# Kernel tuning notes

Hardware: AMD Instinct MI355X
Metric: run time of the kernel (lower is better)

## Reference

```python
import jax, jax.numpy as jnp
import numpy as np

B, C, T = 8, 512, 2048
INTER = C // 2            # inter_channels default = in_channels // 2
L = 2                     # temporal_layer_num


def _pos_encoding(c, t):
    # standard sinusoidal PE, returned as (c, t) to match pos().permute(0,2,1)
    pos = jnp.arange(t, dtype=jnp.float32)[:, None]            # (t,1)
    i = jnp.arange(0, c, 2, dtype=jnp.float32)                 # (c/2,)
    div = jnp.exp(-(jnp.log(10000.0) / c) * i)                 # (c/2,)
    pe = jnp.zeros((t, c), dtype=jnp.float32)
    pe = pe.at[:, 0::2].set(jnp.sin(pos * div))
    pe = pe.at[:, 1::2].set(jnp.cos(pos * div))
    return pe.T                                                # (c,t)


def _conv1x1(w, b, x):
    # kernel_size=1 Conv1d == channel GEMM: w (o,c), x (b,c,t) -> (b,o,t)
    return jnp.einsum('oc,bct->bot', w, x) + b[:, None]


def _temporal_conv(x, w, d):
    # Conv2d(1, c, kernel=(3, c), dilation=(d,1), padding=(d,0), no bias)
    # x (b,c,t) -> input (b,1,t,c); kernel w (c,3,c) -> (c,1,3,c); out (b,c,t,1)
    x4 = x.transpose(0, 2, 1)[:, None, :, :]
    k = w[:, None, :, :]
    y = jax.lax.conv_general_dilated(
        x4, k, window_strides=(1, 1), padding=((d, d), (0, 0)),
        rhs_dilation=(d, 1), dimension_numbers=('NCHW', 'OIHW', 'NCHW'))
    return y[..., 0]                                           # (b,c,t)


def setup_inputs() -> dict:
    key = jax.random.key(0)
    ks = jax.random.split(key, 12)
    n = lambda k, shape, s=0.02: jax.random.normal(k, shape, jnp.float32) * s
    return {
        'x': jax.random.normal(ks[0], (B, C, T), jnp.float32),
        'w_tr': n(ks[1], (C, C)),
        'b_tr': jnp.zeros((C,), jnp.float32),
        'w_tc': n(ks[2], (L, C, 3, C), 0.001),   # init.normal_(std=0.001)
        'w_g': n(ks[3], (L + 1, INTER, C)),
        'b_g': jnp.zeros((L + 1, INTER), jnp.float32),
        'w_th': n(ks[4], (L + 1, INTER, C)),
        'b_th': jnp.zeros((L + 1, INTER), jnp.float32),
        'w_ph': n(ks[5], (L + 1, INTER, C)),
        'b_ph': jnp.zeros((L + 1, INTER), jnp.float32),
        'w_W': n(ks[6], (C, INTER * (L + 1))),
        'b_W': jnp.zeros((C,), jnp.float32),
        'gamma': 1.0 + n(ks[7], (C,)),
        'beta': n(ks[8], (C,)),
    }


def reference(x, w_tr, b_tr, w_tc, w_g, b_g, w_th, b_th, w_ph, b_ph,
              w_W, b_W, gamma, beta):
    b, c, t = x.shape
    x = x + _pos_encoding(c, t)[None]                 # add positional encoding
    x = jax.nn.relu(_conv1x1(w_tr, b_tr, x))          # tranpos_w + relu

    # temporal dilated-conv features, then raw x as last branch
    temps = [_temporal_conv(x, w_tc[i], i + 1) for i in range(w_tc.shape[0])]
    temps.append(x)

    ys = []
    for i, tx in enumerate(temps):
        gx = _conv1x1(w_g[i], b_g[i], tx)             # (b,inter,t)
        th = _conv1x1(w_th[i], b_th[i], tx)           # (b,inter,t)
        ph = _conv1x1(w_ph[i], b_ph[i], tx)           # (b,inter,t)
        f = jax.nn.softmax(jnp.einsum('bit,bis->bts', th, ph), axis=-1)
        ys.append(jnp.einsum('bts,bis->bit', f, gx))  # (b,inter,t)

    y = jnp.concatenate(ys, axis=1)                   # (b, 3*inter, t)
    wy = _conv1x1(w_W, b_W, y)                        # (b,c,t)
    # BatchNorm1d, training-mode batch stats over (batch, time)
    mean = wy.mean(axis=(0, 2), keepdims=True)
    var = wy.var(axis=(0, 2), keepdims=True)
    wy = (wy - mean) * jax.lax.rsqrt(var + 1e-5)
    wy = wy * gamma[None, :, None] + beta[None, :, None]
    return wy + x
```

## Files before the change

### kernel.cpp

```cpp
#include <hip/hip_runtime.h>

#define B_ 8
#define C_ 512
#define T_ 2048
#define I_ 256

typedef _Float16 f16x8 __attribute__((ext_vector_type(8)));
typedef float f32x4 __attribute__((ext_vector_type(4)));
typedef unsigned short u16;
typedef unsigned short u16x4 __attribute__((ext_vector_type(4)));

__device__ __forceinline__ u16 f2h(float f) {
    _Float16 h = (_Float16)f;
    return *(u16*)&h;
}
__device__ __forceinline__ float h2f(u16 u) {
    _Float16 h = *(_Float16*)&u;
    return (float)h;
}

#define AS1 __attribute__((address_space(1)))
#define AS3 __attribute__((address_space(3)))
__device__ __forceinline__ void gload16(const u16* g, u16* l) {
    __builtin_amdgcn_global_load_lds((const AS1 void*)(const void*)g,
                                     (AS3 void*)(void*)l, 16, 0, 0);
}

template <int WMODE, bool BIAS, bool RELU>
__global__ __launch_bounds__(256) void mfma_gemm(
    const u16* __restrict__ A, long aB, int aZdiv, int lda,
    const u16* __restrict__ Bm, long bB, int ldb,
    const float* __restrict__ bias, int biasStride,
    float* __restrict__ Cf, u16* __restrict__ Cn, long cB, int ldc,
    u16* __restrict__ Ct, long ctB, int ldct, int ctOff,
    int K)
{
    __shared__ u16 sA[128 * 64];
    __shared__ u16 sB[128 * 64];
    const int z = blockIdx.z;
    const int zw = z / aZdiv;
    const int m0 = blockIdx.y * 128, n0 = blockIdx.x * 128;
    const int tid = threadIdx.x;
    const int lane = tid & 63, wv = tid >> 6;
    const int wm = wv >> 1, wn = wv & 1;
    const int l15 = lane & 15, l4 = lane >> 4;

    const u16* Ab = A + (long)zw * aB + (long)m0 * lda;
    const u16* Bb = Bm + (long)z * bB + (long)n0 * ldb;

    const int srow = wv * 32 + (lane >> 3);
    const int sk16 = (lane & 7) ^ (lane >> 3);

    f32x4 acc[4][4];
    #pragma unroll
    for (int i = 0; i < 4; ++i)
        #pragma unroll
        for (int j = 0; j < 4; ++j) acc[i][j] = (f32x4){0.f, 0.f, 0.f, 0.f};

    for (int k0 = 0; k0 < K; k0 += 64) {
        #pragma unroll
        for (int ch = 0; ch < 4; ++ch) {
            gload16(Ab + (long)(srow + ch * 8) * lda + k0 + sk16 * 8,
                    &sA[wv * 2048 + ch * 512]);
            gload16(Bb + (long)(srow + ch * 8) * ldb + k0 + sk16 * 8,
                    &sB[wv * 2048 + ch * 512]);
        }
        __syncthreads();
        #pragma unroll
        for (int kk = 0; kk < 2; ++kk) {
            f16x8 af[4], bfr[4];
            #pragma unroll
            for (int f = 0; f < 4; ++f) {
                const int ra = wm * 64 + f * 16 + l15;
                af[f] = *(const f16x8*)&sA[ra * 64 + ((((kk << 2) | l4) ^ (ra & 7)) << 3)];
                const int rb = wn * 64 + f * 16 + l15;
                bfr[f] = *(const f16x8*)&sB[rb * 64 + ((((kk << 2) | l4) ^ (rb & 7)) << 3)];
            }
            #pragma unroll
            for (int mi = 0; mi < 4; ++mi)
                #pragma unroll
                for (int ni = 0; ni < 4; ++ni)
                    acc[mi][ni] = __builtin_amdgcn_mfma_f32_16x16x32_f16(
                        af[mi], bfr[ni], acc[mi][ni], 0, 0, 0);
        }
        __syncthreads();
    }

    #pragma unroll
    for (int mi = 0; mi < 4; ++mi) {
        const int mb = m0 + wm * 64 + mi * 16 + l4 * 4;
        float bv[4] = {0.f, 0.f, 0.f, 0.f};
        if (BIAS) {
            const float* bp = bias + (long)zw * biasStride;
            #pragma unroll
            for (int r = 0; r < 4; ++r) bv[r] = bp[mb + r];
        }
        #pragma unroll
        for (int ni = 0; ni < 4; ++ni) {
            const int nb = n0 + wn * 64 + ni * 16 + l15;
            float v[4];
            #pragma unroll
            for (int r = 0; r < 4; ++r) {
                v[r] = acc[mi][ni][r] + bv[r];
                if (RELU) v[r] = fmaxf(v[r], 0.f);
            }
            if (WMODE & 1) {
                #pragma unroll
                for (int r = 0; r < 4; ++r)
                    Cf[(long)z * cB + (long)(mb + r) * ldc + nb] = v[r];
            }
            if (WMODE & 2) {
                #pragma unroll
                for (int r = 0; r < 4; ++r)
                    Cn[(long)z * cB + (long)(mb + r) * ldc + nb] = f2h(v[r]);
            }
            if (WMODE & 4) {
                u16x4 pk;
                #pragma unroll
                for (int r = 0; r < 4; ++r) pk[r] = f2h(v[r]);
                *(u16x4*)&Ct[(long)z * ctB + (long)nb * ldct + ctOff + mb] = pk;
            }
        }
    }
}

__global__ __launch_bounds__(512) void flash_attn(
    const u16* __restrict__ thA, const u16* __restrict__ phA,
    const u16* __restrict__ gxA, u16* __restrict__ YT)
{
    __shared__ u16 sK[64 * 256];
    __shared__ u16 sV[256 * 64];
    __shared__ u16 sP[8 * 16 * 64];

    const int flat = blockIdx.y * 16 + blockIdx.x;
    const int swz = (flat & 7) * 48 + (flat >> 3);
    const int qb = swz & 15, z = swz >> 4;
    const int br = z >> 3, b = z & 7;
    const int t0 = qb * 128;
    const int tid = threadIdx.x;
    const int lane = tid & 63, wv = tid >> 6;
    const int l15 = lane & 15, l4 = lane >> 4;

    const u16* Qz = thA + (long)z * (T_ * I_);
    const u16* Kz = phA + (long)z * (T_ * I_);
    const u16* Vz = gxA + (long)z * ((long)I_ * T_);

    f16x8 qf[8];
    {
        const u16* qrow = Qz + (long)(t0 + wv * 16 + l15) * I_ + l4 * 8;
        #pragma unroll
        for (int ks = 0; ks < 8; ++ks) qf[ks] = *(const f16x8*)(qrow + ks * 32);
    }

    f32x4 oacc[16];
    #pragma unroll
    for (int i = 0; i < 16; ++i) oacc[i] = (f32x4){0.f, 0.f, 0.f, 0.f};
    float mrun[4] = {-1e30f, -1e30f, -1e30f, -1e30f};
    float lrun[4] = {0.f, 0.f, 0.f, 0.f};

    const int krow = tid >> 5;
    const int kk16 = (tid & 31) ^ (krow & 7);
    const int vrow = tid >> 3;
    const int vk16 = (tid & 7) ^ (vrow & 7);

    for (int s0 = 0; s0 < T_; s0 += 64) {
        #pragma unroll
        for (int is = 0; is < 4; ++is) {
            gload16(Kz + (long)(s0 + is * 16 + krow) * I_ + kk16 * 8,
                    &sK[is * 4096 + tid * 8]);
            gload16(Vz + (long)(is * 64 + vrow) * T_ + s0 + vk16 * 8,
                    &sV[is * 4096 + tid * 8]);
        }
        __syncthreads();

        f32x4 sacc[4];
        #pragma unroll
        for (int nf = 0; nf < 4; ++nf) sacc[nf] = (f32x4){0.f, 0.f, 0.f, 0.f};
        #pragma unroll
        for (int nf = 0; nf < 4; ++nf) {
            const int srow = nf * 16 + l15;
            #pragma unroll
            for (int ks = 0; ks < 8; ++ks) {
                f16x8 kf = *(const f16x8*)&sK[srow * 256 + ((((ks << 2) | l4) ^ (srow & 7)) << 3)];
                sacc[nf] = __builtin_amdgcn_mfma_f32_16x16x32_f16(qf[ks], kf, sacc[nf], 0, 0, 0);
            }
        }

        float scale[4];
        #pragma unroll
        for (int r = 0; r < 4; ++r) {
            float v0 = fmaxf(fmaxf(sacc[0][r], sacc[1][r]),
                             fmaxf(sacc[2][r], sacc[3][r]));
            #pragma unroll
            for (int o = 8; o; o >>= 1) v0 = fmaxf(v0, __shfl_xor(v0, o, 64));
            const float mnew = fmaxf(mrun[r], v0);
            scale[r] = __expf(mrun[r] - mnew);
            mrun[r] = mnew;
        }
        float rsum[4] = {0.f, 0.f, 0.f, 0.f};
        #pragma unroll
        for (int nf = 0; nf < 4; ++nf) {
            #pragma unroll
            for (int r = 0; r < 4; ++r) {
                const float p = __expf(sacc[nf][r] - mrun[r]);
                rsum[r] += p;
                const int tl = l4 * 4 + r;
                const int sl = l15 + nf * 16;
                sP[wv * 1024 + tl * 64 + ((((sl >> 3) ^ (tl & 7)) << 3) | (sl & 7))] = f2h(p);
            }
        }
        #pragma unroll
        for (int r = 0; r < 4; ++r) {
            #pragma unroll
            for (int o = 8; o; o >>= 1) rsum[r] += __shfl_xor(rsum[r], o, 64);
            lrun[r] = lrun[r] * scale[r] + rsum[r];
        }
        #pragma unroll
        for (int nf = 0; nf < 16; ++nf)
            #pragma unroll
            for (int r = 0; r < 4; ++r) oacc[nf][r] *= scale[r];

        f16x8 pa[2];
        #pragma unroll
        for (int kk = 0; kk < 2; ++kk)
            pa[kk] = *(const f16x8*)&sP[wv * 1024 + l15 * 64 + ((((kk << 2) | l4) ^ (l15 & 7)) << 3)];
        #pragma unroll
        for (int nf = 0; nf < 16; ++nf) {
            const int dvr = nf * 16 + l15;
            #pragma unroll
            for (int kk = 0; kk < 2; ++kk) {
                f16x8 vf = *(const f16x8*)&sV[dvr * 64 + ((((kk << 2) | l4) ^ (dvr & 7)) << 3)];
                oacc[nf] = __builtin_amdgcn_mfma_f32_16x16x32_f16(pa[kk], vf, oacc[nf], 0, 0, 0);
            }
        }
        __syncthreads();
    }

    #pragma unroll
    for (int r = 0; r < 4; ++r) {
        const float inv = 1.f / lrun[r];
        const int t = t0 + wv * 16 + l4 * 4 + r;
        u16* dst = YT + ((long)b * T_ + t) * (3 * I_) + br * I_ + l15;
        #pragma unroll
        for (int nf = 0; nf < 16; ++nf)
            dst[nf * 16] = f2h(oacc[nf][r] * inv);
    }
}

__global__ __launch_bounds__(256) void to_f16(
    const float* __restrict__ s, u16* __restrict__ d, long n4)
{
    const long i = (long)blockIdx.x * 256 + threadIdx.x;
    if (i >= n4) return;
    const float4 v = ((const float4*)s)[i];
    u16x4 pk = {f2h(v.x), f2h(v.y), f2h(v.z), f2h(v.w)};
    ((u16x4*)d)[i] = pk;
}

__global__ __launch_bounds__(256) void peT_kernel(float* __restrict__ peT)
{
    const int idx = blockIdx.x * 256 + threadIdx.x;
    const int c = idx & (C_ - 1), t = idx >> 9;
    const float i2 = (float)(c & ~1);
    const float freq = expf(-(9.210340371976184f / (float)C_) * i2);
    const float ang = (float)t * freq;
    peT[idx] = (c & 1) ? cosf(ang) : sinf(ang);
}

__global__ __launch_bounds__(256) void xpose_add(
    const float* __restrict__ x, const float* __restrict__ peT,
    u16* __restrict__ xpeT)
{
    __shared__ float tile[64][65];
    const int b = blockIdx.z;
    const int t0 = blockIdx.x * 64, c0 = blockIdx.y * 64;
    const int rr = threadIdx.x >> 4, cc4 = (threadIdx.x & 15) << 2;
    #pragma unroll
    for (int p = 0; p < 4; ++p) {
        const int row = rr + p * 16;
        const float4 v = *(const float4*)&x[((long)b * C_ + c0 + row) * T_ + t0 + cc4];
        tile[row][cc4 + 0] = v.x; tile[row][cc4 + 1] = v.y;
        tile[row][cc4 + 2] = v.z; tile[row][cc4 + 3] = v.w;
    }
    __syncthreads();
    #pragma unroll
    for (int p = 0; p < 4; ++p) {
        const int tt = rr + p * 16;
        const int gt = t0 + tt;
        const float4 pv = *(const float4*)&peT[(long)gt * C_ + c0 + cc4];
        u16x4 pk = {f2h(tile[cc4 + 0][tt] + pv.x),
                    f2h(tile[cc4 + 1][tt] + pv.y),
                    f2h(tile[cc4 + 2][tt] + pv.z),
                    f2h(tile[cc4 + 3][tt] + pv.w)};
        *(u16x4*)&xpeT[((long)b * T_ + gt) * C_ + c0 + cc4] = pk;
    }
}

__global__ __launch_bounds__(256) void build_bpt(
    const u16* __restrict__ x1T, u16* __restrict__ BpT, int d)
{
    const long i8 = (long)blockIdx.x * 256 + threadIdx.x;
    const long flat = i8 << 3;
    const int col = (int)(flat % (3 * C_));
    const long rest = flat / (3 * C_);
    const int t = (int)(rest & (T_ - 1));
    const int b = (int)(rest >> 11);
    const int kh = col >> 9;
    const int c = col & (C_ - 1);
    const int ts = t + (kh - 1) * d;
    uint4 v = make_uint4(0u, 0u, 0u, 0u);
    if ((unsigned)ts < (unsigned)T_)
        v = *(const uint4*)&x1T[((long)b * T_ + ts) * C_ + c];
    *(uint4*)&BpT[flat] = v;
}

__global__ __launch_bounds__(256) void stats_kernel(
    const float* __restrict__ wy, float* __restrict__ mean,
    float* __restrict__ rstd)
{
    __shared__ float sm[8];
    const int o = blockIdx.x, tid = threadIdx.x;
    float s = 0.f, ss = 0.f;
    for (int idx = tid; idx < B_ * T_; idx += 256) {
        const int b = idx >> 11, t = idx & (T_ - 1);
        const float vv = wy[((long)b * C_ + o) * T_ + t];
        s += vv; ss += vv * vv;
    }
    #pragma unroll
    for (int off = 32; off; off >>= 1) {
        s += __shfl_xor(s, off, 64);
        ss += __shfl_xor(ss, off, 64);
    }
    if ((tid & 63) == 0) { sm[tid >> 6] = s; sm[4 + (tid >> 6)] = ss; }
    __syncthreads();
    if (tid == 0) {
        s = sm[0] + sm[1] + sm[2] + sm[3];
        ss = sm[4] + sm[5] + sm[6] + sm[7];
        const float mu = s / (float)(B_ * T_);
        const float var = ss / (float)(B_ * T_) - mu * mu;
        mean[o] = mu;
        rstd[o] = rsqrtf(var + 1e-5f);
    }
}

__global__ __launch_bounds__(256) void final_kernel(
    float* __restrict__ out, const u16* __restrict__ x1n,
    const float* __restrict__ mean, const float* __restrict__ rstd,
    const float* __restrict__ gamma, const float* __restrict__ beta)
{
    const long i4 = (long)blockIdx.x * 256 + threadIdx.x;
    const long i = i4 * 4;
    const int c = (int)((i / T_) & (C_ - 1));
    const float4 w = ((const float4*)out)[i4];
    const uint2 xv = ((const uint2*)x1n)[i4];
    const u16* xb = (const u16*)&xv;
    const float mu = mean[c];
    const float a = rstd[c] * gamma[c];
    const float bb = beta[c];
    float4 r;
    r.x = (w.x - mu) * a + bb + h2f(xb[0]);
    r.y = (w.y - mu) * a + bb + h2f(xb[1]);
    r.z = (w.z - mu) * a + bb + h2f(xb[2]);
    r.w = (w.w - mu) * a + bb + h2f(xb[3]);
    ((float4*)out)[i4] = r;
}

extern "C" void kernel_launch(void* const* d_in, const int* in_sizes, int n_in,
                              void* d_out, int out_size, void* d_ws, size_t ws_size,
                              hipStream_t stream)
{
    const float* x    = (const float*)d_in[0];
    const float* w_tr = (const float*)d_in[1];
    const float* b_tr = (const float*)d_in[2];
    const float* w_tc = (const float*)d_in[3];
    const float* w_g  = (const float*)d_in[4];
    const float* b_g  = (const float*)d_in[5];
    const float* w_th = (const float*)d_in[6];
    const float* b_th = (const float*)d_in[7];
    const float* w_ph = (const float*)d_in[8];
    const float* b_ph = (const float*)d_in[9];
    const float* w_W  = (const float*)d_in[10];
    const float* b_W  = (const float*)d_in[11];
    const float* gamma = (const float*)d_in[12];
    const float* beta  = (const float*)d_in[13];
    float* out = (float*)d_out;

    char* pp = (char*)d_ws;
    auto nextp = [&](long bytes) { char* r = pp; pp += (bytes + 255) & ~255L; return r; };
    const long TC = (long)T_ * C_;
    const long CT = (long)C_ * T_;
    const long TI = (long)T_ * I_;
    const long IT = (long)I_ * T_;

    float* peT  = (float*)nextp(4L * T_ * C_);
    u16* xpeT   = (u16*)nextp(2L * B_ * TC);
    u16* x1n    = (u16*)nextp(2L * B_ * CT);
    u16* txAll  = (u16*)nextp(2L * 3 * B_ * TC);
    u16* BpT    = (u16*)nextp(2L * B_ * T_ * 3 * C_);
    u16* gxAll  = (u16*)nextp(2L * 3 * B_ * IT);
    u16* thAll  = (u16*)nextp(2L * 3 * B_ * TI);
    u16* phAll  = (u16*)nextp(2L * 3 * B_ * TI);
    u16* YT     = (u16*)nextp(2L * B_ * T_ * 3 * I_);
    u16* w_trb  = (u16*)nextp(2L * C_ * C_);
    u16* w_tcb  = (u16*)nextp(2L * 2 * C_ * 3 * C_);
    u16* w_gb   = (u16*)nextp(2L * 3 * I_ * C_);
    u16* w_thb  = (u16*)nextp(2L * 3 * I_ * C_);
    u16* w_phb  = (u16*)nextp(2L * 3 * I_ * C_);
    u16* w_Wb   = (u16*)nextp(2L * C_ * 3 * I_);
    float* meanb = (float*)nextp(4L * C_);
    float* rstdb = (float*)nextp(4L * C_);

    u16* x1T = txAll + 2L * B_ * TC;

    auto cvt = [&](const float* s, u16* d, long n) {
        to_f16<<<(int)((n / 4 + 255) / 256), 256, 0, stream>>>(s, d, n / 4);
    };
    cvt(w_tr, w_trb, (long)C_ * C_);
    cvt(w_tc, w_tcb, 2L * C_ * 3 * C_);
    cvt(w_g,  w_gb,  3L * I_ * C_);
    cvt(w_th, w_thb, 3L * I_ * C_);
    cvt(w_ph, w_phb, 3L * I_ * C_);
    cvt(w_W,  w_Wb,  (long)C_ * 3 * I_);

    peT_kernel<<<(T_ * C_) / 256, 256, 0, stream>>>(peT);
    xpose_add<<<dim3(T_ / 64, C_ / 64, B_), 256, 0, stream>>>(x, peT, xpeT);

    mfma_gemm<6, true, true><<<dim3(16, 4, 8), 256, 0, stream>>>(
        w_trb, 0, 1, C_, xpeT, TC, C_, b_tr, 0,
        nullptr, x1n, CT, T_, x1T, TC, C_, 0, C_);

    build_bpt<<<(int)(B_ * T_ * 3 * C_ / 8 / 256), 256, 0, stream>>>(x1T, BpT, 1);
    mfma_gemm<4, false, false><<<dim3(16, 4, 8), 256, 0, stream>>>(
        w_tcb, 0, 1, 3 * C_, BpT, 3 * TC, 3 * C_, nullptr, 0,
        nullptr, nullptr, 0, 0, txAll, TC, C_, 0, 3 * C_);
    build_bpt<<<(int)(B_ * T_ * 3 * C_ / 8 / 256), 256, 0, stream>>>(x1T, BpT, 2);
    mfma_gemm<4, false, false><<<dim3(16, 4, 8), 256, 0, stream>>>(
        w_tcb + (long)C_ * 3 * C_, 0, 1, 3 * C_, BpT, 3 * TC, 3 * C_, nullptr, 0,
        nullptr, nullptr, 0, 0, txAll + (long)B_ * TC, TC, C_, 0, 3 * C_);

    mfma_gemm<2, true, false><<<dim3(16, 2, 24), 256, 0, stream>>>(
        w_gb, (long)I_ * C_, 8, C_, txAll, TC, C_, b_g, I_,
        nullptr, gxAll, IT, T_, nullptr, 0, 0, 0, C_);
    mfma_gemm<4, true, false><<<dim3(16, 2, 24), 256, 0, stream>>>(
        w_thb, (long)I_ * C_, 8, C_, txAll, TC, C_, b_th, I_,
        nullptr, nullptr, 0, 0, thAll, TI, I_, 0, C_);
    mfma_gemm<4, true, false><<<dim3(16, 2, 24), 256, 0, stream>>>(
        w_phb, (long)I_ * C_, 8, C_, txAll, TC, C_, b_ph, I_,
        nullptr, nullptr, 0, 0, phAll, TI, I_, 0, C_);

    flash_attn<<<dim3(16, 24), 512, 0, stream>>>(thAll, phAll, gxAll, YT);

    mfma_gemm<1, true, false><<<dim3(16, 4, 8), 256, 0, stream>>>(
        w_Wb, 0, 1, 3 * I_, YT, 3 * TI, 3 * I_, b_W, 0,
        out, nullptr, CT, T_, nullptr, 0, 0, 0, 3 * I_);

    stats_kernel<<<C_, 256, 0, stream>>>(out, meanb, rstdb);
    final_kernel<<<(int)(B_ * C_ * T_ / 4 / 256), 256, 0, stream>>>(
        out, x1n, meanb, rstdb, gamma, beta);
}
```

Baseline: 539.9 us.

## Fuse im2col into temporal-conv GEMM via padded slabs; widen flash-attn per-wave rows

The dilated temporal conv no longer materializes a 3x-wide im2col buffer (build_bpt). The GEMM instead reads row-shifted tiles straight from a zero-padded (T+4)-row x1 slab, and every activation buffer moves to that padded layout. Flash attention drops to 256 threads, with each wave handling 32 query rows so each K/V fragment feeds two MFMAs. It also gains setprio hints and a launch bound that allows two blocks per CU. The cost is higher register pressure in attention and an extra memset for the padding.

```diff
diff --git a/kernel.cpp b/kernel.cpp
--- a/kernel.cpp
+++ b/kernel.cpp
@@ -4,6 +4,7 @@
 #define C_ 512
 #define T_ 2048
 #define I_ 256
+#define TP_ (T_ + 4)
 
 typedef _Float16 f16x8 __attribute__((ext_vector_type(8)));
 typedef float f32x4 __attribute__((ext_vector_type(4)));
@@ -26,14 +27,14 @@
                                      (AS3 void*)(void*)l, 16, 0, 0);
 }
 
-template <int WMODE, bool BIAS, bool RELU>
+template <int WMODE, bool BIAS, bool RELU, bool TCONV>
 __global__ __launch_bounds__(256) void mfma_gemm(
     const u16* __restrict__ A, long aB, int aZdiv, int lda,
     const u16* __restrict__ Bm, long bB, int ldb,
     const float* __restrict__ bias, int biasStride,
     float* __restrict__ Cf, u16* __restrict__ Cn, long cB, int ldc,
     u16* __restrict__ Ct, long ctB, int ldct, int ctOff,
-    int K)
+    int K, int dShift)
 {
     __shared__ u16 sA[128 * 64];
     __shared__ u16 sB[128 * 64];
@@ -58,11 +59,18 @@
         for (int j = 0; j < 4; ++j) acc[i][j] = (f32x4){0.f, 0.f, 0.f, 0.f};
 
     for (int k0 = 0; k0 < K; k0 += 64) {
+        int bCol = k0;
+        int rOff = 0;
+        if (TCONV) {
+            const int kh = k0 >> 9;
+            rOff = (kh - 1) * dShift;
+            bCol = k0 & 511;
+        }
         #pragma unroll
         for (int ch = 0; ch < 4; ++ch) {
             gload16(Ab + (long)(srow + ch * 8) * lda + k0 + sk16 * 8,
                     &sA[wv * 2048 + ch * 512]);
-            gload16(Bb + (long)(srow + ch * 8) * ldb + k0 + sk16 * 8,
+            gload16(Bb + (long)(srow + ch * 8 + rOff) * ldb + bCol + sk16 * 8,
                     &sB[wv * 2048 + ch * 512]);
         }
         __syncthreads();
@@ -124,13 +132,13 @@
     }
 }
 
-__global__ __launch_bounds__(512) void flash_attn(
+__global__ __launch_bounds__(256, 2) void flash_attn(
     const u16* __restrict__ thA, const u16* __restrict__ phA,
     const u16* __restrict__ gxA, u16* __restrict__ YT)
 {
     __shared__ u16 sK[64 * 256];
     __shared__ u16 sV[256 * 64];
-    __shared__ u16 sP[8 * 16 * 64];
+    __shared__ u16 sP[4 * 32 * 64];
 
     const int flat = blockIdx.y * 16 + blockIdx.x;
     const int swz = (flat & 7) * 48 + (flat >> 3);
@@ -145,106 +153,126 @@
     const u16* Kz = phA + (long)z * (T_ * I_);
     const u16* Vz = gxA + (long)z * ((long)I_ * T_);
 
-    f16x8 qf[8];
-    {
-        const u16* qrow = Qz + (long)(t0 + wv * 16 + l15) * I_ + l4 * 8;
-        #pragma unroll
-        for (int ks = 0; ks < 8; ++ks) qf[ks] = *(const f16x8*)(qrow + ks * 32);
-    }
-
-    f32x4 oacc[16];
-    #pragma unroll
-    for (int i = 0; i < 16; ++i) oacc[i] = (f32x4){0.f, 0.f, 0.f, 0.f};
-    float mrun[4] = {-1e30f, -1e30f, -1e30f, -1e30f};
-    float lrun[4] = {0.f, 0.f, 0.f, 0.f};
-
-    const int krow = tid >> 5;
-    const int kk16 = (tid & 31) ^ (krow & 7);
-    const int vrow = tid >> 3;
-    const int vk16 = (tid & 7) ^ (vrow & 7);
+    f16x8 qf[2][8];
+    #pragma unroll
+    for (int m = 0; m < 2; ++m) {
+        const u16* qrow = Qz + (long)(t0 + wv * 32 + m * 16 + l15) * I_ + l4 * 8;
+        #pragma unroll
+        for (int ks = 0; ks < 8; ++ks) qf[m][ks] = *(const f16x8*)(qrow + ks * 32);
+    }
+
+    f32x4 oacc[2][16];
+    #pragma unroll
+    for (int m = 0; m < 2; ++m)
+        #pragma unroll
+        for (int i = 0; i < 16; ++i) oacc[m][i] = (f32x4){0.f, 0.f, 0.f, 0.f};
+    float mrun[2][4], lrun[2][4];
+    #pragma unroll
+    for (int m = 0; m < 2; ++m)
+        #pragma unroll
+        for (int r = 0; r < 4; ++r) { mrun[m][r] = -1e30f; lrun[m][r] = 0.f; }
 
     for (int s0 = 0; s0 < T_; s0 += 64) {
         #pragma unroll
-        for (int is = 0; is < 4; ++is) {
-            gload16(Kz + (long)(s0 + is * 16 + krow) * I_ + kk16 * 8,
-                    &sK[is * 4096 + tid * 8]);
-            gload16(Vz + (long)(is * 64 + vrow) * T_ + s0 + vk16 * 8,
-                    &sV[is * 4096 + tid * 8]);
+        for (int rr = 0; rr < 8; ++rr) {
+            const int fk = rr * 256 + tid;
+            const int ksr = fk >> 5, kslot = fk & 31;
+            gload16(Kz + (long)(s0 + ksr) * I_ + ((kslot ^ (ksr & 7)) << 3),
+                    &sK[fk * 8]);
+            const int dv = fk >> 3, vslot = fk & 7;
+            gload16(Vz + (long)dv * T_ + s0 + ((vslot ^ (dv & 7)) << 3),
+                    &sV[fk * 8]);
         }
         __syncthreads();
 
-        f32x4 sacc[4];
-        #pragma unroll
-        for (int nf = 0; nf < 4; ++nf) sacc[nf] = (f32x4){0.f, 0.f, 0.f, 0.f};
+        f32x4 sacc[2][4];
+        #pragma unroll
+        for (int m = 0; m < 2; ++m)
+            #pragma unroll
+            for (int nf = 0; nf < 4; ++nf) sacc[m][nf] = (f32x4){0.f, 0.f, 0.f, 0.f};
+        __builtin_amdgcn_s_setprio(1);
         #pragma unroll
         for (int nf = 0; nf < 4; ++nf) {
             const int srow = nf * 16 + l15;
             #pragma unroll
             for (int ks = 0; ks < 8; ++ks) {
                 f16x8 kf = *(const f16x8*)&sK[srow * 256 + ((((ks << 2) | l4) ^ (srow & 7)) << 3)];
-                sacc[nf] = __builtin_amdgcn_mfma_f32_16x16x32_f16(qf[ks], kf, sacc[nf], 0, 0, 0);
-            }
-        }
-
-        float scale[4];
-        #pragma unroll
-        for (int r = 0; r < 4; ++r) {
-            float v0 = fmaxf(fmaxf(sacc[0][r], sacc[1][r]),
-                             fmaxf(sacc[2][r], sacc[3][r]));
-            #pragma unroll
-            for (int o = 8; o; o >>= 1) v0 = fmaxf(v0, __shfl_xor(v0, o, 64));
-            const float mnew = fmaxf(mrun[r], v0);
-            scale[r] = __expf(mrun[r] - mnew);
-            mrun[r] = mnew;
-        }
-        float rsum[4] = {0.f, 0.f, 0.f, 0.f};
-        #pragma unroll
-        for (int nf = 0; nf < 4; ++nf) {
+                sacc[0][nf] = __builtin_amdgcn_mfma_f32_16x16x32_f16(qf[0][ks], kf, sacc[0][nf], 0, 0, 0);
+                sacc[1][nf] = __builtin_amdgcn_mfma_f32_16x16x32_f16(qf[1][ks], kf, sacc[1][nf], 0, 0, 0);
+            }
+        }
+        __builtin_amdgcn_s_setprio(0);
+
+        #pragma unroll
+        for (int m = 0; m < 2; ++m) {
+            float scale[4];
             #pragma unroll
             for (int r = 0; r < 4; ++r) {
-                const float p = __expf(sacc[nf][r] - mrun[r]);
-                rsum[r] += p;
-                const int tl = l4 * 4 + r;
-                const int sl = l15 + nf * 16;
-                sP[wv * 1024 + tl * 64 + ((((sl >> 3) ^ (tl & 7)) << 3) | (sl & 7))] = f2h(p);
-            }
-        }
-        #pragma unroll
-        for (int r = 0; r < 4; ++r) {
-            #pragma unroll
-            for (int o = 8; o; o >>= 1) rsum[r] += __shfl_xor(rsum[r], o, 64);
-            lrun[r] = lrun[r] * scale[r] + rsum[r];
-        }
-        #pragma unroll
-        for (int nf = 0; nf < 16; ++nf)
-            #pragma unroll
-            for (int r = 0; r < 4; ++r) oacc[nf][r] *= scale[r];
-
-        f16x8 pa[2];
-        #pragma unroll
-        for (int kk = 0; kk < 2; ++kk)
-            pa[kk] = *(const f16x8*)&sP[wv * 1024 + l15 * 64 + ((((kk << 2) | l4) ^ (l15 & 7)) << 3)];
+                float v0 = fmaxf(fmaxf(sacc[m][0][r], sacc[m][1][r]),
+                                 fmaxf(sacc[m][2][r], sacc[m][3][r]));
+                #pragma unroll
+                for (int o = 8; o; o >>= 1) v0 = fmaxf(v0, __shfl_xor(v0, o, 64));
+                const float mnew = fmaxf(mrun[m][r], v0);
+                scale[r] = __expf(mrun[m][r] - mnew);
+                mrun[m][r] = mnew;
+            }
+            float rsum[4] = {0.f, 0.f, 0.f, 0.f};
+            #pragma unroll
+            for (int nf = 0; nf < 4; ++nf) {
+                #pragma unroll
+                for (int r = 0; r < 4; ++r) {
+                    const float p = __expf(sacc[m][nf][r] - mrun[m][r]);
+                    rsum[r] += p;
+                    const int tl = m * 16 + l4 * 4 + r;
+                    const int sl = l15 + nf * 16;
+                    sP[wv * 2048 + tl * 64 + ((((sl >> 3) ^ (tl & 7)) << 3) | (sl & 7))] = f2h(p);
+                }
+            }
+            #pragma unroll
+            for (int r = 0; r < 4; ++r) {
+                #pragma unroll
+                for (int o = 8; o; o >>= 1) rsum[r] += __shfl_xor(rsum[r], o, 64);
+                lrun[m][r] = lrun[m][r] * scale[r] + rsum[r];
+            }
+            #pragma unroll
+            for (int nf = 0; nf < 16; ++nf)
+                #pragma unroll
+                for (int r = 0; r < 4; ++r) oacc[m][nf][r] *= scale[r];
+        }
+
+        f16x8 pa[2][2];
+        #pragma unroll
+        for (int m = 0; m < 2; ++m)
+            #pragma unroll
+            for (int kk = 0; kk < 2; ++kk)
+                pa[m][kk] = *(const f16x8*)&sP[wv * 2048 + (m * 16 + l15) * 64 +
+                                               ((((kk << 2) | l4) ^ (l15 & 7)) << 3)];
+        __builtin_amdgcn_s_setprio(1);
         #pragma unroll
         for (int nf = 0; nf < 16; ++nf) {
             const int dvr = nf * 16 + l15;
             #pragma unroll
             for (int kk = 0; kk < 2; ++kk) {
                 f16x8 vf = *(const f16x8*)&sV[dvr * 64 + ((((kk << 2) | l4) ^ (dvr & 7)) << 3)];
-                oacc[nf] = __builtin_amdgcn_mfma_f32_16x16x32_f16(pa[kk], vf, oacc[nf], 0, 0, 0);
-            }
-        }
+                oacc[0][nf] = __builtin_amdgcn_mfma_f32_16x16x32_f16(pa[0][kk], vf, oacc[0][nf], 0, 0, 0);
+                oacc[1][nf] = __builtin_amdgcn_mfma_f32_16x16x32_f16(pa[1][kk], vf, oacc[1][nf], 0, 0, 0);
+            }
+        }
+        __builtin_amdgcn_s_setprio(0);
         __syncthreads();
     }
 
     #pragma unroll
-    for (int r = 0; r < 4; ++r) {
-        const float inv = 1.f / lrun[r];
-        const int t = t0 + wv * 16 + l4 * 4 + r;
-        u16* dst = YT + ((long)b * T_ + t) * (3 * I_) + br * I_ + l15;
-        #pragma unroll
-        for (int nf = 0; nf < 16; ++nf)
-            dst[nf * 16] = f2h(oacc[nf][r] * inv);
-    }
+    for (int m = 0; m < 2; ++m)
+        #pragma unroll
+        for (int r = 0; r < 4; ++r) {
+            const float inv = 1.f / lrun[m][r];
+            const int t = t0 + wv * 32 + m * 16 + l4 * 4 + r;
+            u16* dst = YT + ((long)b * T_ + t) * (3 * I_) + br * I_ + l15;
+            #pragma unroll
+            for (int nf = 0; nf < 16; ++nf)
+                dst[nf * 16] = f2h(oacc[m][nf][r] * inv);
+        }
 }
 
 __global__ __launch_bounds__(256) void to_f16(
@@ -294,24 +322,6 @@
                     f2h(tile[cc4 + 3][tt] + pv.w)};
         *(u16x4*)&xpeT[((long)b * T_ + gt) * C_ + c0 + cc4] = pk;
     }
-}
-
-__global__ __launch_bounds__(256) void build_bpt(
-    const u16* __restrict__ x1T, u16* __restrict__ BpT, int d)
-{
-    const long i8 = (long)blockIdx.x * 256 + threadIdx.x;
-    const long flat = i8 << 3;
-    const int col = (int)(flat % (3 * C_));
-    const long rest = flat / (3 * C_);
-    const int t = (int)(rest & (T_ - 1));
-    const int b = (int)(rest >> 11);
-    const int kh = col >> 9;
-    const int c = col & (C_ - 1);
-    const int ts = t + (kh - 1) * d;
-    uint4 v = make_uint4(0u, 0u, 0u, 0u);
-    if ((unsigned)ts < (unsigned)T_)
-        v = *(const uint4*)&x1T[((long)b * T_ + ts) * C_ + c];
-    *(uint4*)&BpT[flat] = v;
 }
 
 __global__ __launch_bounds__(256) void stats_kernel(
@@ -387,16 +397,16 @@
 
     char* pp = (char*)d_ws;
     auto nextp = [&](long bytes) { char* r = pp; pp += (bytes + 255) & ~255L; return r; };
-    const long TC = (long)T_ * C_;
-    const long CT = (long)C_ * T_;
-    const long TI = (long)T_ * I_;
-    const long IT = (long)I_ * T_;
+    const long TC  = (long)T_ * C_;
+    const long CT  = (long)C_ * T_;
+    const long TPC = (long)TP_ * C_;
+    const long TI  = (long)T_ * I_;
+    const long IT  = (long)I_ * T_;
 
     float* peT  = (float*)nextp(4L * T_ * C_);
     u16* xpeT   = (u16*)nextp(2L * B_ * TC);
     u16* x1n    = (u16*)nextp(2L * B_ * CT);
-    u16* txAll  = (u16*)nextp(2L * 3 * B_ * TC);
-    u16* BpT    = (u16*)nextp(2L * B_ * T_ * 3 * C_);
+    u16* txAll  = (u16*)nextp(2L * 3 * B_ * TPC);
     u16* gxAll  = (u16*)nextp(2L * 3 * B_ * IT);
     u16* thAll  = (u16*)nextp(2L * 3 * B_ * TI);
     u16* phAll  = (u16*)nextp(2L * 3 * B_ * TI);
@@ -410,7 +420,9 @@
     float* meanb = (float*)nextp(4L * C_);
     float* rstdb = (float*)nextp(4L * C_);
 
-    u16* x1T = txAll + 2L * B_ * TC;
+    u16* slab0 = txAll;
+    u16* slab1 = txAll + B_ * TPC;
+    u16* slab2 = txAll + 2L * B_ * TPC;
 
     auto cvt = [&](const float* s, u16* d, long n) {
         to_f16<<<(int)((n / 4 + 255) / 256), 256, 0, stream>>>(s, d, n / 4);
@@ -425,34 +437,34 @@
     peT_kernel<<<(T_ * C_) / 256, 256, 0, stream>>>(peT);
     xpose_add<<<dim3(T_ / 64, C_ / 64, B_), 256, 0, stream>>>(x, peT, xpeT);
 
-    mfma_gemm<6, true, true><<<dim3(16, 4, 8), 256, 0, stream>>>(
+    hipMemsetAsync(slab2, 0, 2L * B_ * TPC, stream);
+
+    mfma_gemm<6, true, true, false><<<dim3(16, 4, 8), 256, 0, stream>>>(
         w_trb, 0, 1, C_, xpeT, TC, C_, b_tr, 0,
-        nullptr, x1n, CT, T_, x1T, TC, C_, 0, C_);
-
-    build_bpt<<<(int)(B_ * T_ * 3 * C_ / 8 / 256), 256, 0, stream>>>(x1T, BpT, 1);
-    mfma_gemm<4, false, false><<<dim3(16, 4, 8), 256, 0, stream>>>(
-        w_tcb, 0, 1, 3 * C_, BpT, 3 * TC, 3 * C_, nullptr, 0,
-        nullptr, nullptr, 0, 0, txAll, TC, C_, 0, 3 * C_);
-    build_bpt<<<(int)(B_ * T_ * 3 * C_ / 8 / 256), 256, 0, stream>>>(x1T, BpT, 2);
-    mfma_gemm<4, false, false><<<dim3(16, 4, 8), 256, 0, stream>>>(
-        w_tcb + (long)C_ * 3 * C_, 0, 1, 3 * C_, BpT, 3 * TC, 3 * C_, nullptr, 0,
-        nullptr, nullptr, 0, 0, txAll + (long)B_ * TC, TC, C_, 0, 3 * C_);
-
-    mfma_gemm<2, true, false><<<dim3(16, 2, 24), 256, 0, stream>>>(
-        w_gb, (long)I_ * C_, 8, C_, txAll, TC, C_, b_g, I_,
-        nullptr, gxAll, IT, T_, nullptr, 0, 0, 0, C_);
-    mfma_gemm<4, true, false><<<dim3(16, 2, 24), 256, 0, stream>>>(
-        w_thb, (long)I_ * C_, 8, C_, txAll, TC, C_, b_th, I_,
-        nullptr, nullptr, 0, 0, thAll, TI, I_, 0, C_);
-    mfma_gemm<4, true, false><<<dim3(16, 2, 24), 256, 0, stream>>>(
-        w_phb, (long)I_ * C_, 8, C_, txAll, TC, C_, b_ph, I_,
-        nullptr, nullptr, 0, 0, phAll, TI, I_, 0, C_);
-
-    flash_attn<<<dim3(16, 24), 512, 0, stream>>>(thAll, phAll, gxAll, YT);
-
-    mfma_gemm<1, true, false><<<dim3(16, 4, 8), 256, 0, stream>>>(
-        w_Wb, 0, 1, 3 * I_, YT, 3 * TI, 3 * I_, b_W, 0,
-        out, nullptr, CT, T_, nullptr, 0, 0, 0, 3 * I_);
+        nullptr, x1n, CT, T_, slab2 + 2 * C_, TPC, C_, 0, C_, 0);
+
+    mfma_gemm<4, false, false, true><<<dim3(16, 4, 8), 256, 0, stream>>>(
+        w_tcb, 0, 1, 3 * C_, slab2 + 2 * C_, TPC, C_, nullptr, 0,
+        nullptr, nullptr, 0, 0, slab0 + 2 * C_, TPC, C_, 0, 3 * C_, 1);
+    mfma_gemm<4, false, false, true><<<dim3(16, 4, 8), 256, 0, stream>>>(
+        w_tcb + (long)C_ * 3 * C_, 0, 1, 3 * C_, slab2 + 2 * C_, TPC, C_, nullptr, 0,
+        nullptr, nullptr, 0, 0, slab1 + 2 * C_, TPC, C_, 0, 3 * C_, 2);
+
+    mfma_gemm<2, true, false, false><<<dim3(16, 2, 24), 256, 0, stream>>>(
+        w_gb, (long)I_ * C_, 8, C_, txAll + 2 * C_, TPC, C_, b_g, I_,
+        nullptr, gxAll, IT, T_, nullptr, 0, 0, 0, C_, 0);
+    mfma_gemm<4, true, false, false><<<dim3(16, 2, 24), 256, 0, stream>>>(
+        w_thb, (long)I_ * C_, 8, C_, txAll + 2 * C_, TPC, C_, b_th, I_,
+        nullptr, nullptr, 0, 0, thAll, TI, I_, 0, C_, 0);
+    mfma_gemm<4, true, false, false><<<dim3(16, 2, 24), 256, 0, stream>>>(
+        w_phb, (long)I_ * C_, 8, C_, txAll + 2 * C_, TPC, C_, b_ph, I_,
+        nullptr, nullptr, 0, 0, phAll, TI, I_, 0, C_, 0);
+
+    flash_attn<<<dim3(16, 24), 256, 0, stream>>>(thAll, phAll, gxAll, YT);
+
+    mfma_gemm<1, true, false, false><<<dim3(16, 4, 8), 256, 0, stream>>>(
+        w_Wb, 0, 1, 3 * I_, YT, (long)T_ * 3 * I_, 3 * I_, b_W, 0,
+        out, nullptr, CT, T_, nullptr, 0, 0, 0, 3 * I_, 0);
 
     stats_kernel<<<C_, 256, 0, stream>>>(out, meanb, rstdb);
     final_kernel<<<(int)(B_ * C_ * T_ / 4 / 256), 256, 0, stream>>>(
```

Result: slower. 997.0 us (+84.7%).
